# Kernel optimization log

Hardware: AMD Instinct MI355X
Metric: run time of the kernel (lower is better)

## Reference

```python
import jax, jax.numpy as jnp
import numpy as np

TEMPERATURE = 8.0
EPS = 1e-8  # torch F.cosine_similarity clamps each norm at eps=1e-8

B, L, H, D = 4, 1024, 8, 64


def setup_inputs() -> dict:
    key = jax.random.key(0)
    kq, kk, kv = jax.random.split(key, 3)
    q = jax.random.normal(kq, (B, L, H, D), dtype=jnp.float32)
    k = jax.random.normal(kk, (B, L, H, D), dtype=jnp.float32)
    v = jax.random.normal(kv, (B, L, H, D), dtype=jnp.float32)
    return {"q": q, "k": k, "v": v}


def _l2_normalize(x):
    # matches torch cosine_similarity: divide by max(||x||, eps)
    n = jnp.sqrt(jnp.sum(x * x, axis=-1, keepdims=True))
    return x / jnp.maximum(n, EPS)


def reference(q, k, v):
    # [B, L, H, D] -> [B, H, L, D]
    qt = jnp.swapaxes(q, 1, 2)
    kt = jnp.swapaxes(k, 1, 2)
    vt = jnpp = jnp.swapaxes(v, 1, 2)
    qn = _l2_normalize(qt)
    kn = _l2_normalize(kt)
    # cosine similarity via matmul instead of O(L*L*D) broadcast
    attn = jnp.einsum("bhid,bhjd->bhij", qn, kn) / TEMPERATURE  # [B,H,L,L]
    attn = jax.nn.softmax(attn, axis=-1)
    out = jnp.einsum("bhij,bhjd->bhid", attn, vt)  # [B,H,L,D]
    return out, attn
```

## Files before the change

kernel.cpp:

```cpp
#include <hip/hip_runtime.h>

#define NB 4
#define NL 1024
#define NH 8
#define ND 64
#define NBH 32

typedef __attribute__((ext_vector_type(8))) short bhalf8;
typedef __attribute__((ext_vector_type(4))) float f32x4;

static __device__ inline unsigned short f2bf(float f) {
    union { float f; unsigned u; } x; x.f = f;
    unsigned r = x.u + 0x7FFFu + ((x.u >> 16) & 1u);
    return (unsigned short)(r >> 16);
}

__global__ __launch_bounds__(256) void norm_qk_kernel(const float* __restrict__ q,
                                                      const float* __restrict__ k,
                                                      unsigned short* __restrict__ qn,
                                                      unsigned short* __restrict__ kn) {
    int wid  = threadIdx.x >> 6;
    int lane = threadIdx.x & 63;
    int r = blockIdx.x * 4 + wid;
    int b = r >> 13;
    int l = (r >> 3) & (NL - 1);
    int h = r & (NH - 1);

    float qv = q[(size_t)r * ND + lane];
    float kv = k[(size_t)r * ND + lane];
    float qs = qv * qv, ks = kv * kv;
    #pragma unroll
    for (int m = 1; m < 64; m <<= 1) {
        qs += __shfl_xor(qs, m);
        ks += __shfl_xor(ks, m);
    }
    float qd = 1.0f / (fmaxf(sqrtf(qs), 1e-8f) * 5.545177444479562f);
    float kd = 1.0f / fmaxf(sqrtf(ks), 1e-8f);

    size_t o = ((size_t)(b * NH + h) * NL + l) * ND + lane;
    qn[o] = f2bf(qv * qd);
    kn[o] = f2bf(kv * kd);
}

__global__ __launch_bounds__(1024) void vtrans_kernel(const float* __restrict__ v,
                                                      unsigned short* __restrict__ vt) {
    __shared__ float tile[64 * 65];
    int bh = blockIdx.x;
    int b = bh >> 3, h = bh & 7;
    int l0 = blockIdx.y * 64;
    int wid = threadIdx.x >> 6, lane = threadIdx.x & 63;

    #pragma unroll
    for (int rr = 0; rr < 4; ++rr) {
        int row = wid * 4 + rr;
        float val = v[(((size_t)b * NL + l0 + row) * NH + h) * ND + lane];
        tile[lane * 65 + row] = val;
    }
    __syncthreads();
    #pragma unroll
    for (int dd = 0; dd < 4; ++dd) {
        int d = wid * 4 + dd;
        vt[((size_t)(bh * ND + d)) * NL + l0 + lane] = f2bf(tile[d * 65 + lane]);
    }
}

__global__ __launch_bounds__(256) void attn_kernel(const unsigned short* __restrict__ qn,
                                                   const unsigned short* __restrict__ kn,
                                                   const unsigned short* __restrict__ vt,
                                                   float* __restrict__ outp,
                                                   float* __restrict__ attnp) {
    __shared__ __align__(16) unsigned char smem_raw[4 * 16 * 66 * 4];
    __shared__ float dred[4][16];
    __shared__ float invd[16];

    unsigned short* ptile = (unsigned short*)smem_raw;
    float*          oaccf = (float*)smem_raw;

    int bh   = blockIdx.x;
    int wid  = threadIdx.x >> 6;
    int lane = threadIdx.x & 63;
    int c    = lane & 15;
    int quad = lane >> 4;
    int m0   = blockIdx.y * 16;

    unsigned short* myp = ptile + wid * (16 * 40);

    const unsigned short* qbase = qn + ((size_t)(bh * NL + m0 + c)) * ND + quad * 8;
    bhalf8 qa0 = *(const bhalf8*)(qbase);
    bhalf8 qa1 = *(const bhalf8*)(qbase + 32);

    const unsigned short* kbh = kn + (size_t)bh * NL * ND;

    float denom[4] = {0.f, 0.f, 0.f, 0.f};
    for (int jt = 0; jt < 16; ++jt) {
        int j0 = wid * 256 + jt * 16;
        const unsigned short* kb = kbh + ((size_t)(j0 + c)) * ND + quad * 8;
        bhalf8 kf0 = *(const bhalf8*)(kb);
        bhalf8 kf1 = *(const bhalf8*)(kb + 32);
        f32x4 s = {0.f, 0.f, 0.f, 0.f};
        s = __builtin_amdgcn_mfma_f32_16x16x32_bf16(qa0, kf0, s, 0, 0, 0);
        s = __builtin_amdgcn_mfma_f32_16x16x32_bf16(qa1, kf1, s, 0, 0, 0);
        #pragma unroll
        for (int r = 0; r < 4; ++r) denom[r] += __builtin_amdgcn_exp2f(s[r]);
    }
    #pragma unroll
    for (int r = 0; r < 4; ++r) {
        float d = denom[r];
        d += __shfl_xor(d, 1);
        d += __shfl_xor(d, 2);
        d += __shfl_xor(d, 4);
        d += __shfl_xor(d, 8);
        denom[r] = d;
    }
    if (c == 0) {
        #pragma unroll
        for (int r = 0; r < 4; ++r) dred[wid][quad * 4 + r] = denom[r];
    }
    __syncthreads();
    if (threadIdx.x < 16) {
        invd[threadIdx.x] = 1.0f / (dred[0][threadIdx.x] + dred[1][threadIdx.x] +
                                    dred[2][threadIdx.x] + dred[3][threadIdx.x]);
    }
    __syncthreads();
    float inv[4];
    #pragma unroll
    for (int r = 0; r < 4; ++r) inv[r] = invd[quad * 4 + r];

    float* attnrow = attnp + ((size_t)(bh * NL + m0)) * NL;
    const unsigned short* vbh = vt + (size_t)bh * ND * NL;

    f32x4 o[4] = {{0.f,0.f,0.f,0.f},{0.f,0.f,0.f,0.f},{0.f,0.f,0.f,0.f},{0.f,0.f,0.f,0.f}};
    for (int j2 = 0; j2 < 8; ++j2) {
        int jb = wid * 256 + j2 * 32;
        #pragma unroll
        for (int sub = 0; sub < 2; ++sub) {
            int j0 = jb + sub * 16;
            const unsigned short* kb = kbh + ((size_t)(j0 + c)) * ND + quad * 8;
            bhalf8 kf0 = *(const bhalf8*)(kb);
            bhalf8 kf1 = *(const bhalf8*)(kb + 32);
            f32x4 s = {0.f, 0.f, 0.f, 0.f};
            s = __builtin_amdgcn_mfma_f32_16x16x32_bf16(qa0, kf0, s, 0, 0, 0);
            s = __builtin_amdgcn_mfma_f32_16x16x32_bf16(qa1, kf1, s, 0, 0, 0);
            #pragma unroll
            for (int r = 0; r < 4; ++r) {
                float a = __builtin_amdgcn_exp2f(s[r]) * inv[r];
                attnrow[(size_t)(quad * 4 + r) * NL + j0 + c] = a;
                myp[(quad * 4 + r) * 40 + sub * 16 + c] = f2bf(a);
            }
        }
        bhalf8 pa = *(const bhalf8*)(myp + c * 40 + quad * 8);
        #pragma unroll
        for (int nt = 0; nt < 4; ++nt) {
            const unsigned short* vb = vbh + (size_t)(nt * 16 + c) * NL + jb + quad * 8;
            bhalf8 vf = *(const bhalf8*)(vb);
            o[nt] = __builtin_amdgcn_mfma_f32_16x16x32_bf16(pa, vf, o[nt], 0, 0, 0);
        }
    }

    __syncthreads();
    #pragma unroll
    for (int nt = 0; nt < 4; ++nt) {
        #pragma unroll
        for (int r = 0; r < 4; ++r) {
            oaccf[wid * 1056 + (quad * 4 + r) * 66 + nt * 16 + c] = o[nt][r];
        }
    }
    __syncthreads();
    float* obase = outp + ((size_t)(bh * NL + m0)) * ND;
    #pragma unroll
    for (int i = 0; i < 4; ++i) {
        int e = i * 256 + threadIdx.x;
        int row = e >> 6, col = e & 63;
        float s = oaccf[row * 66 + col] + oaccf[1056 + row * 66 + col] +
                  oaccf[2112 + row * 66 + col] + oaccf[3168 + row * 66 + col];
        obase[e] = s;
    }
}

extern "C" void kernel_launch(void* const* d_in, const int* in_sizes, int n_in,
                              void* d_out, int out_size, void* d_ws, size_t ws_size,
                              hipStream_t stream) {
    const float* q = (const float*)d_in[0];
    const float* k = (const float*)d_in[1];
    const float* v = (const float*)d_in[2];

    float* outp  = (float*)d_out;
    float* attnp = outp + (size_t)NB * NH * NL * ND;

    unsigned short* qn = (unsigned short*)d_ws;
    unsigned short* kn = qn + (size_t)NB * NH * NL * ND;
    unsigned short* vt = kn + (size_t)NB * NH * NL * ND;

    norm_qk_kernel<<<(NB * NL * NH) / 4, 256, 0, stream>>>(q, k, qn, kn);
    vtrans_kernel<<<dim3(NBH, NL / 64), 1024, 0, stream>>>(v, vt);
    attn_kernel<<<dim3(NBH, NL / 16), 256, 0, stream>>>(qn, kn, vt, outp, attnp);
}
```

Before: 236.8 us.

## Fuse prep kernels, vectorize loads, and cache exp scores in registers

Merges the q/k normalization and v transpose into one launch and switches both to float4 loads and ushort4 stores. In the attention kernel, the exponentiated scores from the first pass are kept in a 64-float register array, so the second pass no longer reloads K and recomputes the QK MFMAs and exp. This saves a kernel launch, some memory traffic and half the QK compute. The cost is higher register pressure from s[16] plus full unrolling, which may lower occupancy.

Measured after the change: 207.6 us. 1.14x faster.

```diff
diff --git a/kernel.cpp b/kernel.cpp
--- a/kernel.cpp
+++ b/kernel.cpp
@@ -15,52 +15,60 @@
     return (unsigned short)(r >> 16);
 }
 
-__global__ __launch_bounds__(256) void norm_qk_kernel(const float* __restrict__ q,
-                                                      const float* __restrict__ k,
-                                                      unsigned short* __restrict__ qn,
-                                                      unsigned short* __restrict__ kn) {
-    int wid  = threadIdx.x >> 6;
-    int lane = threadIdx.x & 63;
-    int r = blockIdx.x * 4 + wid;
-    int b = r >> 13;
-    int l = (r >> 3) & (NL - 1);
-    int h = r & (NH - 1);
-
-    float qv = q[(size_t)r * ND + lane];
-    float kv = k[(size_t)r * ND + lane];
-    float qs = qv * qv, ks = kv * kv;
-    #pragma unroll
-    for (int m = 1; m < 64; m <<= 1) {
-        qs += __shfl_xor(qs, m);
-        ks += __shfl_xor(ks, m);
-    }
-    float qd = 1.0f / (fmaxf(sqrtf(qs), 1e-8f) * 5.545177444479562f);
-    float kd = 1.0f / fmaxf(sqrtf(ks), 1e-8f);
-
-    size_t o = ((size_t)(b * NH + h) * NL + l) * ND + lane;
-    qn[o] = f2bf(qv * qd);
-    kn[o] = f2bf(kv * kd);
-}
-
-__global__ __launch_bounds__(1024) void vtrans_kernel(const float* __restrict__ v,
-                                                      unsigned short* __restrict__ vt) {
-    __shared__ float tile[64 * 65];
-    int bh = blockIdx.x;
-    int b = bh >> 3, h = bh & 7;
-    int l0 = blockIdx.y * 64;
-    int wid = threadIdx.x >> 6, lane = threadIdx.x & 63;
-
-    #pragma unroll
-    for (int rr = 0; rr < 4; ++rr) {
-        int row = wid * 4 + rr;
-        float val = v[(((size_t)b * NL + l0 + row) * NH + h) * ND + lane];
-        tile[lane * 65 + row] = val;
-    }
-    __syncthreads();
-    #pragma unroll
-    for (int dd = 0; dd < 4; ++dd) {
-        int d = wid * 4 + dd;
-        vt[((size_t)(bh * ND + d)) * NL + l0 + lane] = f2bf(tile[d * 65 + lane]);
+__global__ __launch_bounds__(256) void prep_kernel(const float* __restrict__ q,
+                                                   const float* __restrict__ k,
+                                                   const float* __restrict__ v,
+                                                   unsigned short* __restrict__ qn,
+                                                   unsigned short* __restrict__ kn,
+                                                   unsigned short* __restrict__ vt) {
+    int tid = threadIdx.x;
+    if (blockIdx.x < 2048) {
+        int w = tid >> 6, lane = tid & 63;
+        int rowg = blockIdx.x * 16 + w * 4 + (lane >> 4);
+        int c = lane & 15;
+        float4 q4 = ((const float4*)q)[(size_t)rowg * 16 + c];
+        float4 k4 = ((const float4*)k)[(size_t)rowg * 16 + c];
+        float qs = q4.x*q4.x + q4.y*q4.y + q4.z*q4.z + q4.w*q4.w;
+        float ks = k4.x*k4.x + k4.y*k4.y + k4.z*k4.z + k4.w*k4.w;
+        #pragma unroll
+        for (int m = 1; m < 16; m <<= 1) {
+            qs += __shfl_xor(qs, m);
+            ks += __shfl_xor(ks, m);
+        }
+        float qd = 1.0f / (fmaxf(sqrtf(qs), 1e-8f) * 5.545177444479562f);
+        float kd = 1.0f / fmaxf(sqrtf(ks), 1e-8f);
+        int b = rowg >> 13, l = (rowg >> 3) & (NL - 1), h = rowg & (NH - 1);
+        size_t o = ((size_t)(b * NH + h) * NL + l) * 16 + c;
+        ushort4 qo, ko;
+        qo.x = f2bf(q4.x * qd); qo.y = f2bf(q4.y * qd);
+        qo.z = f2bf(q4.z * qd); qo.w = f2bf(q4.w * qd);
+        ko.x = f2bf(k4.x * kd); ko.y = f2bf(k4.y * kd);
+        ko.z = f2bf(k4.z * kd); ko.w = f2bf(k4.w * kd);
+        ((ushort4*)qn)[o] = qo;
+        ((ushort4*)kn)[o] = ko;
+    } else {
+        __shared__ unsigned short tile_t[64 * 68];
+        int bid = blockIdx.x - 2048;
+        int bh = bid >> 4;
+        int b = bh >> 3, h = bh & 7;
+        int l0 = (bid & 15) * 64;
+        #pragma unroll
+        for (int i = 0; i < 4; ++i) {
+            int l = (tid >> 4) + i * 16;
+            int c4 = tid & 15;
+            float4 vv = ((const float4*)v)[(((size_t)b * NL + l0 + l) * NH + h) * 16 + c4];
+            tile_t[(c4 * 4 + 0) * 68 + l] = f2bf(vv.x);
+            tile_t[(c4 * 4 + 1) * 68 + l] = f2bf(vv.y);
+            tile_t[(c4 * 4 + 2) * 68 + l] = f2bf(vv.z);
+            tile_t[(c4 * 4 + 3) * 68 + l] = f2bf(vv.w);
+        }
+        __syncthreads();
+        int d = tid >> 2, lg = tid & 3;
+        #pragma unroll
+        for (int i = 0; i < 4; ++i) {
+            ushort4 u4 = *(const ushort4*)&tile_t[d * 68 + i * 16 + lg * 4];
+            ((ushort4*)vt)[((size_t)(bh * ND + d)) * (NL / 4) + l0 / 4 + i * 4 + lg] = u4;
+        }
     }
 }
 
@@ -91,17 +99,23 @@
 
     const unsigned short* kbh = kn + (size_t)bh * NL * ND;
 
+    f32x4 s[16];
     float denom[4] = {0.f, 0.f, 0.f, 0.f};
+    #pragma unroll
     for (int jt = 0; jt < 16; ++jt) {
         int j0 = wid * 256 + jt * 16;
         const unsigned short* kb = kbh + ((size_t)(j0 + c)) * ND + quad * 8;
         bhalf8 kf0 = *(const bhalf8*)(kb);
         bhalf8 kf1 = *(const bhalf8*)(kb + 32);
-        f32x4 s = {0.f, 0.f, 0.f, 0.f};
-        s = __builtin_amdgcn_mfma_f32_16x16x32_bf16(qa0, kf0, s, 0, 0, 0);
-        s = __builtin_amdgcn_mfma_f32_16x16x32_bf16(qa1, kf1, s, 0, 0, 0);
-        #pragma unroll
-        for (int r = 0; r < 4; ++r) denom[r] += __builtin_amdgcn_exp2f(s[r]);
+        f32x4 acc = {0.f, 0.f, 0.f, 0.f};
+        acc = __builtin_amdgcn_mfma_f32_16x16x32_bf16(qa0, kf0, acc, 0, 0, 0);
+        acc = __builtin_amdgcn_mfma_f32_16x16x32_bf16(qa1, kf1, acc, 0, 0, 0);
+        #pragma unroll
+        for (int r = 0; r < 4; ++r) {
+            float e = __builtin_amdgcn_exp2f(acc[r]);
+            s[jt][r] = e;
+            denom[r] += e;
+        }
     }
     #pragma unroll
     for (int r = 0; r < 4; ++r) {
@@ -130,20 +144,15 @@
     const unsigned short* vbh = vt + (size_t)bh * ND * NL;
 
     f32x4 o[4] = {{0.f,0.f,0.f,0.f},{0.f,0.f,0.f,0.f},{0.f,0.f,0.f,0.f},{0.f,0.f,0.f,0.f}};
+    #pragma unroll
     for (int j2 = 0; j2 < 8; ++j2) {
         int jb = wid * 256 + j2 * 32;
         #pragma unroll
         for (int sub = 0; sub < 2; ++sub) {
             int j0 = jb + sub * 16;
-            const unsigned short* kb = kbh + ((size_t)(j0 + c)) * ND + quad * 8;
-            bhalf8 kf0 = *(const bhalf8*)(kb);
-            bhalf8 kf1 = *(const bhalf8*)(kb + 32);
-            f32x4 s = {0.f, 0.f, 0.f, 0.f};
-            s = __builtin_amdgcn_mfma_f32_16x16x32_bf16(qa0, kf0, s, 0, 0, 0);
-            s = __builtin_amdgcn_mfma_f32_16x16x32_bf16(qa1, kf1, s, 0, 0, 0);
             #pragma unroll
             for (int r = 0; r < 4; ++r) {
-                float a = __builtin_amdgcn_exp2f(s[r]) * inv[r];
+                float a = s[j2 * 2 + sub][r] * inv[r];
                 attnrow[(size_t)(quad * 4 + r) * NL + j0 + c] = a;
                 myp[(quad * 4 + r) * 40 + sub * 16 + c] = f2bf(a);
             }
@@ -171,9 +180,9 @@
     for (int i = 0; i < 4; ++i) {
         int e = i * 256 + threadIdx.x;
         int row = e >> 6, col = e & 63;
-        float s = oaccf[row * 66 + col] + oaccf[1056 + row * 66 + col] +
-                  oaccf[2112 + row * 66 + col] + oaccf[3168 + row * 66 + col];
-        obase[e] = s;
+        float sum = oaccf[row * 66 + col] + oaccf[1056 + row * 66 + col] +
+                    oaccf[2112 + row * 66 + col] + oaccf[3168 + row * 66 + col];
+        obase[e] = sum;
     }
 }
 
@@ -191,7 +200,6 @@
     unsigned short* kn = qn + (size_t)NB * NH * NL * ND;
     unsigned short* vt = kn + (size_t)NB * NH * NL * ND;
 
-    norm_qk_kernel<<<(NB * NL * NH) / 4, 256, 0, stream>>>(q, k, qn, kn);
-    vtrans_kernel<<<dim3(NBH, NL / 64), 1024, 0, stream>>>(v, vt);
+    prep_kernel<<<2048 + 512, 256, 0, stream>>>(q, k, v, qn, kn, vt);
     attn_kernel<<<dim3(NBH, NL / 16), 256, 0, stream>>>(qn, kn, vt, outp, attnp);
 }
```
